# Kernel tuning notes

Measured on AMD Instinct MI355X. Metric: run time of the kernel, lower is better.

The kernel has to match this reference:

```python
import jax, jax.numpy as jnp
import numpy as np

B, S, D, H = 2, 2048, 2048, 16
HD = D // H  # 128


def _rope(x):
    # x: [b, h, s, d] -- standard half-split rotary embedding, theta=10000
    b, h, s, d = x.shape
    inv_freq = 1.0 / (10000.0 ** (jnp.arange(0, d, 2, dtype=jnp.float32) / d))  # [d/2]
    ang = jnp.arange(s, dtype=jnp.float32)[:, None] * inv_freq[None, :]  # [s, d/2]
    cos = jnp.cos(ang)[None, None].astype(x.dtype)
    sin = jnp.sin(ang)[None, None].astype(x.dtype)
    x1, x2 = x[..., : d // 2], x[..., d // 2 :]
    return jnp.concatenate([x1 * cos - x2 * sin, x2 * cos + x1 * sin], axis=-1)


def setup_inputs() -> dict:
    key = jax.random.key(0)
    ks = jax.random.split(key, 11)
    sc = 0.02
    return {
        "queries": jax.random.normal(ks[0], (B, S, D), jnp.float32),
        "keys": jax.random.normal(ks[1], (B, S, D), jnp.float32),
        "values": jax.random.normal(ks[2], (B, S, D), jnp.float32),
        "Wq": jax.random.normal(ks[3], (D, D), jnp.float32) * sc,
        "bq": jax.random.normal(ks[4], (D,), jnp.float32) * sc,
        "Wk": jax.random.normal(ks[5], (D, D), jnp.float32) * sc,
        "bk": jax.random.normal(ks[6], (D,), jnp.float32) * sc,
        "Wv": jax.random.normal(ks[7], (D, D), jnp.float32) * sc,
        "bv": jax.random.normal(ks[8], (D,), jnp.float32) * sc,
        "Wo": jax.random.normal(ks[9], (D, D), jnp.float32) * sc,
        "bo": jax.random.normal(ks[10], (D,), jnp.float32) * sc,
    }


def reference(queries, keys, values, Wq, bq, Wk, bk, Wv, bv, Wo, bo):
    b, sq, _ = queries.shape
    sk = keys.shape[1]
    # projections, split heads: [b, h, s, hd]
    q = (queries @ Wq + bq).reshape(b, sq, H, HD).transpose(0, 2, 1, 3)
    k = (keys @ Wk + bk).reshape(b, sk, H, HD).transpose(0, 2, 1, 3)
    v = (values @ Wv + bv).reshape(b, sk, H, HD).transpose(0, 2, 1, 3)
    q = _rope(q)
    k = _rope(k)
    scores = jnp.einsum("bhqd,bhkd->bhqk", q, k) / jnp.sqrt(jnp.asarray(HD, q.dtype))
    causal = jnp.triu(jnp.ones((sq, sk), dtype=bool), k=1)
    scores = jnp.where(causal, -jnp.inf, scores)
    attn = jax.nn.softmax(scores, axis=-1)
    out = jnp.einsum("bhqk,bhkd->bhqd", attn, v)
    out = out.transpose(0, 2, 1, 3).reshape(b, sq, H * HD)
    return out @ Wo + bo
```

## Files before the change

kernel.cpp:

```cpp
#include <hip/hip_runtime.h>
#include <hip/hip_bf16.h>
#include <math.h>

#define S_LEN 2048
#define D_DIM 2048
#define NHEAD 16
#define HD_DIM 128
#define NROWS 4096
#define BSD 8388608

typedef __bf16 bf16x8 __attribute__((ext_vector_type(8)));
typedef float f32x4 __attribute__((ext_vector_type(4)));
typedef unsigned short u16;
typedef unsigned int u32;

__device__ __forceinline__ float bf2f(u16 h) {
    union { u32 u; float f; } v; v.u = ((u32)h) << 16; return v.f;
}
__device__ __forceinline__ u16 f2bf(float f) {
    union { float f; u32 u; } v; v.f = f;
    u32 r = v.u + 0x7fffu + ((v.u >> 16) & 1u);
    return (u16)(r >> 16);
}

__device__ __forceinline__ void gld16(const void* g, void* l) {
    __builtin_amdgcn_global_load_lds((const __attribute__((address_space(1))) void*)g,
                                     (__attribute__((address_space(3))) void*)l,
                                     16, 0, 0);
}

__device__ __forceinline__ bool detect_f32(const void* p) {
    const u16* h = (const u16*)p;
    int sane = 0;
    for (int i = 0; i < 128; i++) {
        const u16 v = h[2 * i];
        const int e = (v >> 7) & 0xFF;
        sane += (int)((e >= 96 && e <= 150) || ((v & 0x7FFF) == 0));
    }
    return sane < 64;
}

__device__ __forceinline__ bf16x8 load8(const void* X, size_t eidx, bool f32) {
    if (!f32) return *(const bf16x8*)((const u16*)X + eidx);
    const float* xf = (const float*)X + eidx;
    const f32x4 a = *(const f32x4*)xf;
    const f32x4 b = *(const f32x4*)(xf + 4);
    bf16x8 r;
    u16* rp = (u16*)&r;
    rp[0] = f2bf(a[0]); rp[1] = f2bf(a[1]); rp[2] = f2bf(a[2]); rp[3] = f2bf(a[3]);
    rp[4] = f2bf(b[0]); rp[5] = f2bf(b[1]); rp[6] = f2bf(b[2]); rp[7] = f2bf(b[3]);
    return r;
}

__device__ __forceinline__ float bload(const void* b, int i, bool f32) {
    return f32 ? ((const float*)b)[i] : bf2f(((const u16*)b)[i]);
}

__global__ __launch_bounds__(256) void fill_k(float* __restrict__ out, float v, int n) {
    const int i = blockIdx.x * 256 + threadIdx.x;
    if (i < n) out[i] = v;
}

__global__ __launch_bounds__(256) void conv_bf16(const void* __restrict__ in,
                                                 u16* __restrict__ out) {
    const bool f32 = detect_f32(in);
    const size_t i = ((size_t)blockIdx.x * 256 + threadIdx.x) << 3;
    if (f32) {
        const f32x4 a = *(const f32x4*)((const float*)in + i);
        const f32x4 b = *(const f32x4*)((const float*)in + i + 4);
        uint4 w;
        w.x = (u32)f2bf(a[0]) | ((u32)f2bf(a[1]) << 16);
        w.y = (u32)f2bf(a[2]) | ((u32)f2bf(a[3]) << 16);
        w.z = (u32)f2bf(b[0]) | ((u32)f2bf(b[1]) << 16);
        w.w = (u32)f2bf(b[2]) | ((u32)f2bf(b[3]) << 16);
        *(uint4*)&out[i] = w;
    } else {
        *(uint4*)&out[i] = *(const uint4*)&((const u16*)in)[i];
    }
}

__global__ __launch_bounds__(256) void transpose_w(const void* __restrict__ W,
                                                   u16* __restrict__ out) {
    __shared__ float tile[64][68];
    const bool f32w = detect_f32(W);
    const int t = threadIdx.x;
    const int r = t >> 4, c4 = (t & 15) << 2;
    const int kb = blockIdx.y << 6, nb = blockIdx.x << 6;
    if (f32w) {
        #pragma unroll
        for (int i = 0; i < 4; i++) {
            const f32x4 v = *(const f32x4*)((const float*)W +
                (size_t)(kb + r + 16 * i) * D_DIM + nb + c4);
            tile[r + 16 * i][c4 + 0] = v[0];
            tile[r + 16 * i][c4 + 1] = v[1];
            tile[r + 16 * i][c4 + 2] = v[2];
            tile[r + 16 * i][c4 + 3] = v[3];
        }
    } else {
        #pragma unroll
        for (int i = 0; i < 4; i++)
            #pragma unroll
            for (int j = 0; j < 4; j++)
                tile[r + 16 * i][c4 + j] =
                    bf2f(((const u16*)W)[(size_t)(kb + r + 16 * i) * D_DIM + nb + c4 + j]);
    }
    __syncthreads();
    #pragma unroll
    for (int i = 0; i < 4; i++) {
        const int n = nb + r + 16 * i;
        u16 pk[4];
        #pragma unroll
        for (int j = 0; j < 4; j++) pk[j] = f2bf(tile[c4 + j][r + 16 * i]);
        *(uint2*)&out[(size_t)n * D_DIM + kb + c4] = *(uint2*)pk;
    }
}

template<int MODE>
__global__ __launch_bounds__(256) void bt_gemm(const void* __restrict__ X,
                                               const u16* __restrict__ WT,
                                               const void* __restrict__ bias,
                                               void* __restrict__ out) {
    __shared__ __align__(16) u16 a_s[128 * 32];
    __shared__ __align__(16) u16 b_s[128 * 32];
    const bool f32x = (MODE == 0) ? detect_f32(X) : false;
    const bool f32b = detect_f32(bias);
    const int t = threadIdx.x;
    const int wave = t >> 6, lane = t & 63;
    const int quad = lane >> 4, m16 = lane & 15;
    const int wm = (wave >> 1) << 6, wn = (wave & 1) << 6;
    const int rowBase = blockIdx.y << 7, colBase = blockIdx.x << 7;
    const int arow = t >> 2, aoff = (t & 3) << 3;

    f32x4 acc[4][4];
    #pragma unroll
    for (int i = 0; i < 4; i++)
        #pragma unroll
        for (int j = 0; j < 4; j++) acc[i][j] = (f32x4){0.f, 0.f, 0.f, 0.f};

    for (int k0 = 0; k0 < D_DIM; k0 += 32) {
        if (MODE == 0) {
            const bf16x8 av0 = load8(X, (size_t)(rowBase + arow) * D_DIM + k0 + aoff, f32x);
            const bf16x8 av1 = load8(X, (size_t)(rowBase + arow + 64) * D_DIM + k0 + aoff, f32x);
            __syncthreads();
            *(bf16x8*)&a_s[arow * 32 + aoff]        = av0;
            *(bf16x8*)&a_s[(arow + 64) * 32 + aoff] = av1;
            gld16(&WT[(size_t)(colBase + arow) * D_DIM + k0 + aoff],      &b_s[t * 8]);
            gld16(&WT[(size_t)(colBase + arow + 64) * D_DIM + k0 + aoff], &b_s[(t + 256) * 8]);
            __syncthreads();
        } else {
            __syncthreads();
            if (MODE == 2) {
                gld16(&((const u16*)X)[(size_t)(rowBase + arow) * D_DIM + k0 + aoff],
                      &a_s[t * 8]);
                gld16(&((const u16*)X)[(size_t)(rowBase + arow + 64) * D_DIM + k0 + aoff],
                      &a_s[(t + 256) * 8]);
            } else {
                const int kg = k0 + aoff, h = kg >> 7, hd = kg & (HD_DIM - 1);
                const int r0 = rowBase + arow, r1 = r0 + 64;
                gld16(&((const u16*)X)[
                    (((size_t)((r0 >> 11) * NHEAD + h)) * S_LEN + (r0 & (S_LEN - 1))) * HD_DIM + hd],
                    &a_s[t * 8]);
                gld16(&((const u16*)X)[
                    (((size_t)((r1 >> 11) * NHEAD + h)) * S_LEN + (r1 & (S_LEN - 1))) * HD_DIM + hd],
                    &a_s[(t + 256) * 8]);
            }
            gld16(&WT[(size_t)(colBase + arow) * D_DIM + k0 + aoff],      &b_s[t * 8]);
            gld16(&WT[(size_t)(colBase + arow + 64) * D_DIM + k0 + aoff], &b_s[(t + 256) * 8]);
            __syncthreads();
        }

        bf16x8 af[4], bf[4];
        #pragma unroll
        for (int mi = 0; mi < 4; mi++)
            af[mi] = *(bf16x8*)&a_s[(wm + mi * 16 + m16) * 32 + quad * 8];
        #pragma unroll
        for (int ni = 0; ni < 4; ni++)
            bf[ni] = *(bf16x8*)&b_s[(wn + ni * 16 + m16) * 32 + quad * 8];
        #pragma unroll
        for (int mi = 0; mi < 4; mi++)
            #pragma unroll
            for (int ni = 0; ni < 4; ni++)
                acc[mi][ni] = __builtin_amdgcn_mfma_f32_16x16x32_bf16(
                    af[mi], bf[ni], acc[mi][ni], 0, 0, 0);
    }

    #pragma unroll
    for (int ni = 0; ni < 4; ni++) {
        const int col = colBase + wn + ni * 16 + m16;
        const float bv = bload(bias, col, f32b);
        const int h = col >> 7, hd = col & (HD_DIM - 1);
        #pragma unroll
        for (int mi = 0; mi < 4; mi++) {
            #pragma unroll
            for (int r = 0; r < 4; r++) {
                const int row = rowBase + wm + mi * 16 + quad * 4 + r;
                const float v = acc[mi][ni][r] + bv;
                if (MODE == 1) {
                    ((float*)out)[(size_t)row * D_DIM + col] = v;
                } else {
                    const int b = row >> 11, s = row & (S_LEN - 1);
                    ((u16*)out)[(((size_t)(b * NHEAD + h)) * S_LEN + s) * HD_DIM + hd] = f2bf(v);
                }
            }
        }
    }
}

__global__ __launch_bounds__(256) void gemm_qkv(const void* __restrict__ X,
                                                const void* __restrict__ W,
                                                const void* __restrict__ bias,
                                                u16* __restrict__ out) {
    __shared__ __align__(16) u16 a_s[64 * 32];
    __shared__ __align__(16) u16 b_s[64 * 40];
    const bool f32x = detect_f32(X);
    const bool f32w = detect_f32(W);
    const bool f32b = detect_f32(bias);
    const int t = threadIdx.x;
    const int wave = t >> 6, lane = t & 63;
    const int quad = lane >> 4, mrow = lane & 15;
    const int rowBase = blockIdx.y * 64;
    const int colBase = blockIdx.x * 64;
    const int srow = t >> 2, soff = (t & 3) << 3;
    const int krow = t >> 3, ncol0 = (t & 7) << 3;

    f32x4 acc0 = {0.f, 0.f, 0.f, 0.f};
    f32x4 acc1 = acc0, acc2 = acc0, acc3 = acc0;

    for (int k0 = 0; k0 < D_DIM; k0 += 32) {
        const bf16x8 av = load8(X, (size_t)(rowBase + srow) * D_DIM + k0 + soff, f32x);
        const bf16x8 wv = load8(W, (size_t)(k0 + krow) * D_DIM + colBase + ncol0, f32w);
        __syncthreads();
        *(bf16x8*)&a_s[srow * 32 + soff] = av;
        const u16* wp = (const u16*)&wv;
        #pragma unroll
        for (int j = 0; j < 8; j++) b_s[(ncol0 + j) * 40 + krow] = wp[j];
        __syncthreads();
        const bf16x8 af  = *(bf16x8*)&a_s[(wave * 16 + mrow) * 32 + (quad << 3)];
        const bf16x8 bf0 = *(bf16x8*)&b_s[(     mrow) * 40 + (quad << 3)];
        const bf16x8 bf1 = *(bf16x8*)&b_s[(16 + mrow) * 40 + (quad << 3)];
        const bf16x8 bf2 = *(bf16x8*)&b_s[(32 + mrow) * 40 + (quad << 3)];
        const bf16x8 bf3 = *(bf16x8*)&b_s[(48 + mrow) * 40 + (quad << 3)];
        acc0 = __builtin_amdgcn_mfma_f32_16x16x32_bf16(af, bf0, acc0, 0, 0, 0);
        acc1 = __builtin_amdgcn_mfma_f32_16x16x32_bf16(af, bf1, acc1, 0, 0, 0);
        acc2 = __builtin_amdgcn_mfma_f32_16x16x32_bf16(af, bf2, acc2, 0, 0, 0);
        acc3 = __builtin_amdgcn_mfma_f32_16x16x32_bf16(af, bf3, acc3, 0, 0, 0);
    }

    const f32x4 accs[4] = {acc0, acc1, acc2, acc3};
    #pragma unroll
    for (int cb = 0; cb < 4; cb++) {
        const int col = colBase + cb * 16 + mrow;
        const float bv = bload(bias, col, f32b);
        const int h = col >> 7, hd = col & (HD_DIM - 1);
        #pragma unroll
        for (int r = 0; r < 4; r++) {
            const int row = rowBase + wave * 16 + quad * 4 + r;
            const int b = row >> 11, s = row & (S_LEN - 1);
            out[(((size_t)(b * NHEAD + h)) * S_LEN + s) * HD_DIM + hd] =
                f2bf(accs[cb][r] + bv);
        }
    }
}

__global__ __launch_bounds__(256) void gemm_o(const u16* __restrict__ A,
                                              const void* __restrict__ W,
                                              const void* __restrict__ bias,
                                              float* __restrict__ out) {
    __shared__ __align__(16) u16 a_s[64 * 32];
    __shared__ __align__(16) u16 b_s[64 * 40];
    const bool f32w = detect_f32(W);
    const bool f32b = detect_f32(bias);
    const int t = threadIdx.x;
    const int wave = t >> 6, lane = t & 63;
    const int quad = lane >> 4, mrow = lane & 15;
    const int rowBase = blockIdx.y * 64;
    const int colBase = blockIdx.x * 64;
    const int srow = t >> 2, soff = (t & 3) << 3;
    const int krow = t >> 3, ncol0 = (t & 7) << 3;

    f32x4 acc0 = {0.f, 0.f, 0.f, 0.f};
    f32x4 acc1 = acc0, acc2 = acc0, acc3 = acc0;

    const int row = rowBase + srow;
    const int rb = row >> 11, rs = row & (S_LEN - 1);

    for (int k0 = 0; k0 < D_DIM; k0 += 32) {
        const int kg = k0 + soff;
        const int h = kg >> 7, hd = kg & (HD_DIM - 1);
        const bf16x8 av = *(const bf16x8*)&A[
            (((size_t)(rb * NHEAD + h)) * S_LEN + rs) * HD_DIM + hd];
        const bf16x8 wv = load8(W, (size_t)(k0 + krow) * D_DIM + colBase + ncol0, f32w);
        __syncthreads();
        *(bf16x8*)&a_s[srow * 32 + soff] = av;
        const u16* wp = (const u16*)&wv;
        #pragma unroll
        for (int j = 0; j < 8; j++) b_s[(ncol0 + j) * 40 + krow] = wp[j];
        __syncthreads();
        const bf16x8 af  = *(bf16x8*)&a_s[(wave * 16 + mrow) * 32 + (quad << 3)];
        const bf16x8 bf0 = *(bf16x8*)&b_s[(     mrow) * 40 + (quad << 3)];
        const bf16x8 bf1 = *(bf16x8*)&b_s[(16 + mrow) * 40 + (quad << 3)];
        const bf16x8 bf2 = *(bf16x8*)&b_s[(32 + mrow) * 40 + (quad << 3)];
        const bf16x8 bf3 = *(bf16x8*)&b_s[(48 + mrow) * 40 + (quad << 3)];
        acc0 = __builtin_amdgcn_mfma_f32_16x16x32_bf16(af, bf0, acc0, 0, 0, 0);
        acc1 = __builtin_amdgcn_mfma_f32_16x16x32_bf16(af, bf1, acc1, 0, 0, 0);
        acc2 = __builtin_amdgcn_mfma_f32_16x16x32_bf16(af, bf2, acc2, 0, 0, 0);
        acc3 = __builtin_amdgcn_mfma_f32_16x16x32_bf16(af, bf3, acc3, 0, 0, 0);
    }

    const f32x4 accs[4] = {acc0, acc1, acc2, acc3};
    #pragma unroll
    for (int cb = 0; cb < 4; cb++) {
        const int col = colBase + cb * 16 + mrow;
        const float bv = bload(bias, col, f32b);
        #pragma unroll
        for (int r = 0; r < 4; r++) {
            const int orow = rowBase + wave * 16 + quad * 4 + r;
            out[(size_t)orow * D_DIM + col] = accs[cb][r] + bv;
        }
    }
}

__global__ __launch_bounds__(256) void rope_k(u16* __restrict__ q, u16* __restrict__ k) {
    const int idx = blockIdx.x * 256 + threadIdx.x;
    u16* p = blockIdx.y ? k : q;
    const int i  = idx & 63;
    const int s  = (idx >> 6) & (S_LEN - 1);
    const int bh = idx >> 17;
    const size_t base = ((size_t)bh * S_LEN + s) * HD_DIM;
    const float inv = __expf((float)i * -0.14391157f);
    const float ang = (float)s * inv;
    const float c = cosf(ang), sn = sinf(ang);
    const float x1 = bf2f(p[base + i]);
    const float x2 = bf2f(p[base + 64 + i]);
    p[base + i]      = f2bf(x1 * c - x2 * sn);
    p[base + 64 + i] = f2bf(x2 * c + x1 * sn);
}

__device__ __forceinline__ int vswz(int d, int blk8) {
    return d * 72 + (((blk8) ^ ((d ^ (d >> 3)) & 7)) << 3);
}

__global__ __launch_bounds__(256, 3) void flash_mfma(const u16* Q,
                                                     const u16* __restrict__ K,
                                                     const u16* __restrict__ V,
                                                     u16* Out) {
    __shared__ __align__(16) u16 k_s[64 * 136];
    __shared__ __align__(16) u16 v_s[128 * 72];
    __shared__ __align__(16) u16 p_s[64 * 72];
    const int t = threadIdx.x;
    const int wave = t >> 6, lane = t & 63;
    const int quad = lane >> 4, m16 = lane & 15;
    const int h = blockIdx.y, b = blockIdx.z;
    const int q0 = (int)(gridDim.x - 1 - blockIdx.x) << 6;
    const size_t bhoff = ((size_t)(b * NHEAD + h)) * S_LEN * HD_DIM;

    #pragma unroll
    for (int i = 0; i < 4; i++) {
        const int chunk = t + 256 * i;
        const int row = chunk >> 4, d0 = (chunk & 15) << 3;
        *(uint4*)&k_s[row * 136 + d0] =
            *(const uint4*)&Q[bhoff + (size_t)(q0 + row) * HD_DIM + d0];
    }
    __syncthreads();
    bf16x8 qf[4];
    #pragma unroll
    for (int kc = 0; kc < 4; kc++)
        qf[kc] = *(bf16x8*)&k_s[(wave * 16 + m16) * 136 + kc * 32 + quad * 8];

    f32x4 o[8];
    #pragma unroll
    for (int i = 0; i < 8; i++) o[i] = (f32x4){0.f, 0.f, 0.f, 0.f};
    f32x4 m_i = {-1e30f, -1e30f, -1e30f, -1e30f};
    f32x4 l_i = {0.f, 0.f, 0.f, 0.f};

    const int row_g0 = q0 + wave * 16 + quad * 4;
    const float scale = 0.08838834764831843f;
    const int nt = (q0 >> 6) + 1;

    const int krow = t >> 4, kd0 = (t & 15) << 3;
    const int dg = t & 15, kvg = t >> 4;
    const int vsub = (kvg & 1) << 2;

    uint4 kreg[4], vreg[4];
    #pragma unroll
    for (int i = 0; i < 4; i++) {
        kreg[i] = *(const uint4*)&K[bhoff + (size_t)(krow + 16 * i) * HD_DIM + kd0];
        vreg[i] = *(const uint4*)&V[bhoff + (size_t)(kvg * 4 + i) * HD_DIM + dg * 8];
    }

    for (int it = 0; it < nt; ++it) {
        const int kb = it << 6;
        __syncthreads();
        #pragma unroll
        for (int i = 0; i < 4; i++)
            *(uint4*)&k_s[(krow + 16 * i) * 136 + kd0] = kreg[i];
        {
            const u16* v0 = (const u16*)&vreg[0];
            const u16* v1 = (const u16*)&vreg[1];
            const u16* v2 = (const u16*)&vreg[2];
            const u16* v3 = (const u16*)&vreg[3];
            #pragma unroll
            for (int j = 0; j < 8; j++) {
                const int d = dg * 8 + j;
                uint2 w;
                w.x = (u32)v0[j] | ((u32)v1[j] << 16);
                w.y = (u32)v2[j] | ((u32)v3[j] << 16);
                *(uint2*)&v_s[vswz(d, kvg >> 1) + vsub] = w;
            }
        }
        __syncthreads();
        if (it + 1 < nt) {
            const int kb2 = kb + 64;
            #pragma unroll
            for (int i = 0; i < 4; i++) {
                kreg[i] = *(const uint4*)&K[bhoff + (size_t)(kb2 + krow + 16 * i) * HD_DIM + kd0];
                vreg[i] = *(const uint4*)&V[bhoff + (size_t)(kb2 + kvg * 4 + i) * HD_DIM + dg * 8];
            }
        }

        f32x4 s[4];
        #pragma unroll
        for (int f = 0; f < 4; f++) s[f] = (f32x4){0.f, 0.f, 0.f, 0.f};
        __builtin_amdgcn_s_setprio(1);
        #pragma unroll
        for (int kc = 0; kc < 4; kc++) {
            #pragma unroll
            for (int f = 0; f < 4; f++) {
                const bf16x8 kf = *(bf16x8*)&k_s[(f * 16 + m16) * 136 + kc * 32 + quad * 8];
                s[f] = __builtin_amdgcn_mfma_f32_16x16x32_bf16(qf[kc], kf, s[f], 0, 0, 0);
            }
        }
        __builtin_amdgcn_s_setprio(0);

        f32x4 mx;
        #pragma unroll
        for (int r = 0; r < 4; r++) {
            float m0 = -1e30f;
            #pragma unroll
            for (int f = 0; f < 4; f++) {
                float a = s[f][r] * scale;
                if (kb + f * 16 + m16 > row_g0 + r) a = -1e30f;
                s[f][r] = a;
                m0 = fmaxf(m0, a);
            }
            mx[r] = m0;
        }
        #pragma unroll
        for (int d = 1; d <= 8; d <<= 1)
            #pragma unroll
            for (int r = 0; r < 4; r++) mx[r] = fmaxf(mx[r], __shfl_xor(mx[r], d));

        f32x4 alpha, rs;
        #pragma unroll
        for (int r = 0; r < 4; r++) {
            const float mn = fmaxf(m_i[r], mx[r]);
            alpha[r] = __expf(m_i[r] - mn);
            m_i[r] = mn;
            float acc = 0.f;
            #pragma unroll
            for (int f = 0; f < 4; f++) {
                s[f][r] = __expf(s[f][r] - mn);
                acc += s[f][r];
            }
            rs[r] = acc;
        }
        #pragma unroll
        for (int d = 1; d <= 8; d <<= 1)
            #pragma unroll
            for (int r = 0; r < 4; r++) rs[r] += __shfl_xor(rs[r], d);
        #pragma unroll
        for (int r = 0; r < 4; r++) l_i[r] = l_i[r] * alpha[r] + rs[r];

        #pragma unroll
        for (int f = 0; f < 4; f++)
            #pragma unroll
            for (int r = 0; r < 4; r++)
                p_s[(wave * 16 + quad * 4 + r) * 72 + f * 16 + m16] = f2bf(s[f][r]);

        #pragma unroll
        for (int n = 0; n < 8; n++) o[n] *= alpha;

        __builtin_amdgcn_s_setprio(1);
        #pragma unroll
        for (int kc = 0; kc < 2; kc++) {
            const bf16x8 pa = *(bf16x8*)&p_s[(wave * 16 + m16) * 72 + kc * 32 + quad * 8];
            #pragma unroll
            for (int n = 0; n < 8; n++) {
                const int d = n * 16 + m16;
                const bf16x8 vb = *(bf16x8*)&v_s[vswz(d, kc * 4 + quad)];
                o[n] = __builtin_amdgcn_mfma_f32_16x16x32_bf16(pa, vb, o[n], 0, 0, 0);
            }
        }
        __builtin_amdgcn_s_setprio(0);
    }

    f32x4 inv;
    #pragma unroll
    for (int r = 0; r < 4; r++) inv[r] = 1.f / l_i[r];
    #pragma unroll
    for (int n = 0; n < 8; n++)
        #pragma unroll
        for (int r = 0; r < 4; r++)
            Out[bhoff + (size_t)(row_g0 + r) * HD_DIM + n * 16 + m16] =
                f2bf(o[n][r] * inv[r]);
}

extern "C" void kernel_launch(void* const* d_in, const int* in_sizes, int n_in,
                              void* d_out, int out_size, void* d_ws, size_t ws_size,
                              hipStream_t stream) {
    float* outf = (float*)d_out;

    bool order_ok = (n_in == 11);
    if (order_ok) {
        const int expect[11] = {8388608, 8388608, 8388608, 4194304, 2048,
                                4194304, 2048, 4194304, 2048, 4194304, 2048};
        for (int i = 0; i < 11; i++) order_ok = order_ok && (in_sizes[i] == expect[i]);
    }
    if (!order_ok) {
        fill_k<<<dim3((out_size + 255) / 256), dim3(256), 0, stream>>>(outf, 50.f, out_size);
        return;
    }
    if (ws_size < (size_t)BSD * sizeof(u16)) {
        fill_k<<<dim3((out_size + 255) / 256), dim3(256), 0, stream>>>(outf, 25.f, out_size);
        return;
    }

    const void* queries = d_in[0];
    const void* keys    = d_in[1];
    const void* values  = d_in[2];
    const void* Wq = d_in[3]; const void* bq = d_in[4];
    const void* Wk = d_in[5]; const void* bk = d_in[6];
    const void* Wv = d_in[7]; const void* bv = d_in[8];
    const void* Wo = d_in[9]; const void* bo = d_in[10];

    u16* Qb = (u16*)d_ws;
    u16* Kb = (u16*)d_out;
    u16* Vb = Kb + BSD;

    const dim3 tb(256);
    const dim3 gr(16384, 2);
    const dim3 gf(S_LEN / 64, NHEAD, 2);

    const size_t need_fast = (size_t)BSD * 2 + (size_t)D_DIM * D_DIM * 2;
    if (ws_size >= need_fast) {
        u16* WT = Qb + BSD;
        u16* XQ = Kb;
        u16* XK = Vb;
        const dim3 gt(32, 32);
        const dim3 gb(16, 32);
        const dim3 gc(4096);

        conv_bf16<<<gc, tb, 0, stream>>>(queries, XQ);
        conv_bf16<<<gc, tb, 0, stream>>>(keys, XK);

        transpose_w<<<gt, tb, 0, stream>>>(Wq, WT);
        bt_gemm<2><<<gb, tb, 0, stream>>>(XQ, WT, bq, Qb);
        transpose_w<<<gt, tb, 0, stream>>>(Wk, WT);
        bt_gemm<2><<<gb, tb, 0, stream>>>(XK, WT, bk, Kb);
        transpose_w<<<gt, tb, 0, stream>>>(Wv, WT);
        bt_gemm<0><<<gb, tb, 0, stream>>>(values, WT, bv, Vb);

        rope_k<<<gr, tb, 0, stream>>>(Qb, Kb);
        flash_mfma<<<gf, tb, 0, stream>>>(Qb, Kb, Vb, Qb);

        transpose_w<<<gt, tb, 0, stream>>>(Wo, WT);
        bt_gemm<1><<<gb, tb, 0, stream>>>(Qb, WT, bo, outf);
    } else {
        const dim3 gg(32, 64);
        gemm_qkv<<<gg, tb, 0, stream>>>(queries, Wq, bq, Qb);
        gemm_qkv<<<gg, tb, 0, stream>>>(keys,    Wk, bk, Kb);
        gemm_qkv<<<gg, tb, 0, stream>>>(values,  Wv, bv, Vb);
        rope_k<<<gr, tb, 0, stream>>>(Qb, Kb);
        flash_mfma<<<gf, tb, 0, stream>>>(Qb, Kb, Vb, Qb);
        gemm_o<<<gg, tb, 0, stream>>>(Qb, Wo, bo, outf);
    }
}
```

Baseline: 926.0 us.

## Batch QKV weight transposes and projections into single z-indexed launches

When the workspace is large enough, the three weight transposes become one launch with a z grid dimension, and the Q/K/V projection GEMMs become one launch that converts f32 inputs inline instead of running separate conversion kernels. This removes several launches and the intermediate bf16 copies of queries and keys, and gives the GPU three times more blocks per launch. It requires extra workspace for all three transposed weights. The A-tile path now loads through registers rather than async global-to-LDS copies, which could cost some latency hiding.

```diff
diff --git a/kernel.cpp b/kernel.cpp
--- a/kernel.cpp
+++ b/kernel.cpp
@@ -79,8 +79,8 @@
     }
 }
 
-__global__ __launch_bounds__(256) void transpose_w(const void* __restrict__ W,
-                                                   u16* __restrict__ out) {
+__device__ __forceinline__ void transpose_body(const void* __restrict__ W,
+                                               u16* __restrict__ out) {
     __shared__ float tile[64][68];
     const bool f32w = detect_f32(W);
     const int t = threadIdx.x;
@@ -112,6 +112,95 @@
         #pragma unroll
         for (int j = 0; j < 4; j++) pk[j] = f2bf(tile[c4 + j][r + 16 * i]);
         *(uint2*)&out[(size_t)n * D_DIM + kb + c4] = *(uint2*)pk;
+    }
+}
+
+__global__ __launch_bounds__(256) void transpose_w(const void* __restrict__ W,
+                                                   u16* __restrict__ out) {
+    transpose_body(W, out);
+}
+
+__global__ __launch_bounds__(256) void transpose_all(const void* __restrict__ W0,
+                                                     const void* __restrict__ W1,
+                                                     const void* __restrict__ W2,
+                                                     u16* __restrict__ out) {
+    const int z = blockIdx.z;
+    const void* W = (z == 0) ? W0 : (z == 1) ? W1 : W2;
+    transpose_body(W, out + (size_t)z * D_DIM * D_DIM);
+}
+
+__global__ __launch_bounds__(256) void qkv_gemm(const void* __restrict__ Xq,
+                                                const void* __restrict__ Xk,
+                                                const void* __restrict__ Xv,
+                                                const u16* __restrict__ WTbase,
+                                                const void* __restrict__ bqp,
+                                                const void* __restrict__ bkp,
+                                                const void* __restrict__ bvp,
+                                                u16* __restrict__ Oq,
+                                                u16* __restrict__ Ok,
+                                                u16* __restrict__ Ov) {
+    __shared__ __align__(16) u16 a_s[128 * 32];
+    __shared__ __align__(16) u16 b_s[128 * 32];
+    const int z = blockIdx.z;
+    const void* X   = (z == 0) ? Xq  : (z == 1) ? Xk  : Xv;
+    const void* bias= (z == 0) ? bqp : (z == 1) ? bkp : bvp;
+    u16* out        = (z == 0) ? Oq  : (z == 1) ? Ok  : Ov;
+    const u16* WT   = WTbase + (size_t)z * D_DIM * D_DIM;
+    const bool f32x = detect_f32(X);
+    const bool f32b = detect_f32(bias);
+    const int t = threadIdx.x;
+    const int wave = t >> 6, lane = t & 63;
+    const int quad = lane >> 4, m16 = lane & 15;
+    const int wm = (wave >> 1) << 6, wn = (wave & 1) << 6;
+    const int rowBase = blockIdx.y << 7, colBase = blockIdx.x << 7;
+    const int arow = t >> 2, aoff = (t & 3) << 3;
+
+    f32x4 acc[4][4];
+    #pragma unroll
+    for (int i = 0; i < 4; i++)
+        #pragma unroll
+        for (int j = 0; j < 4; j++) acc[i][j] = (f32x4){0.f, 0.f, 0.f, 0.f};
+
+    for (int k0 = 0; k0 < D_DIM; k0 += 32) {
+        const bf16x8 av0 = load8(X, (size_t)(rowBase + arow) * D_DIM + k0 + aoff, f32x);
+        const bf16x8 av1 = load8(X, (size_t)(rowBase + arow + 64) * D_DIM + k0 + aoff, f32x);
+        __syncthreads();
+        *(bf16x8*)&a_s[arow * 32 + aoff]        = av0;
+        *(bf16x8*)&a_s[(arow + 64) * 32 + aoff] = av1;
+        gld16(&WT[(size_t)(colBase + arow) * D_DIM + k0 + aoff],      &b_s[t * 8]);
+        gld16(&WT[(size_t)(colBase + arow + 64) * D_DIM + k0 + aoff], &b_s[(t + 256) * 8]);
+        __syncthreads();
+
+        bf16x8 af[4], bfr[4];
+        #pragma unroll
+        for (int mi = 0; mi < 4; mi++)
+            af[mi] = *(bf16x8*)&a_s[(wm + mi * 16 + m16) * 32 + quad * 8];
+        #pragma unroll
+        for (int ni = 0; ni < 4; ni++)
+            bfr[ni] = *(bf16x8*)&b_s[(wn + ni * 16 + m16) * 32 + quad * 8];
+        #pragma unroll
+        for (int mi = 0; mi < 4; mi++)
+            #pragma unroll
+            for (int ni = 0; ni < 4; ni++)
+                acc[mi][ni] = __builtin_amdgcn_mfma_f32_16x16x32_bf16(
+                    af[mi], bfr[ni], acc[mi][ni], 0, 0, 0);
+    }
+
+    #pragma unroll
+    for (int ni = 0; ni < 4; ni++) {
+        const int col = colBase + wn + ni * 16 + m16;
+        const float bv = bload(bias, col, f32b);
+        const int h = col >> 7, hd = col & (HD_DIM - 1);
+        #pragma unroll
+        for (int mi = 0; mi < 4; mi++) {
+            #pragma unroll
+            for (int r = 0; r < 4; r++) {
+                const int row = rowBase + wm + mi * 16 + quad * 4 + r;
+                const int b = row >> 11, s = row & (S_LEN - 1);
+                out[(((size_t)(b * NHEAD + h)) * S_LEN + s) * HD_DIM + hd] =
+                    f2bf(acc[mi][ni][r] + bv);
+            }
+        }
     }
 }
 
@@ -169,19 +258,19 @@
             __syncthreads();
         }
 
-        bf16x8 af[4], bf[4];
+        bf16x8 af[4], bfr[4];
         #pragma unroll
         for (int mi = 0; mi < 4; mi++)
             af[mi] = *(bf16x8*)&a_s[(wm + mi * 16 + m16) * 32 + quad * 8];
         #pragma unroll
         for (int ni = 0; ni < 4; ni++)
-            bf[ni] = *(bf16x8*)&b_s[(wn + ni * 16 + m16) * 32 + quad * 8];
+            bfr[ni] = *(bf16x8*)&b_s[(wn + ni * 16 + m16) * 32 + quad * 8];
         #pragma unroll
         for (int mi = 0; mi < 4; mi++)
             #pragma unroll
             for (int ni = 0; ni < 4; ni++)
                 acc[mi][ni] = __builtin_amdgcn_mfma_f32_16x16x32_bf16(
-                    af[mi], bf[ni], acc[mi][ni], 0, 0, 0);
+                    af[mi], bfr[ni], acc[mi][ni], 0, 0, 0);
     }
 
     #pragma unroll
@@ -541,8 +630,25 @@
     const dim3 gr(16384, 2);
     const dim3 gf(S_LEN / 64, NHEAD, 2);
 
-    const size_t need_fast = (size_t)BSD * 2 + (size_t)D_DIM * D_DIM * 2;
-    if (ws_size >= need_fast) {
+    const size_t wslot = (size_t)D_DIM * D_DIM * 2;
+    const size_t need_fused = (size_t)BSD * 2 + 3 * wslot;
+    const size_t need_fast  = (size_t)BSD * 2 + wslot;
+
+    if (ws_size >= need_fused) {
+        u16* WT = Qb + BSD;
+        const dim3 gt3(32, 32, 3);
+        const dim3 gt(32, 32);
+        const dim3 gq(16, 32, 3);
+        const dim3 gb(16, 32);
+
+        transpose_all<<<gt3, tb, 0, stream>>>(Wq, Wk, Wv, WT);
+        qkv_gemm<<<gq, tb, 0, stream>>>(queries, keys, values, WT,
+                                        bq, bk, bv, Qb, Kb, Vb);
+        transpose_w<<<gt, tb, 0, stream>>>(Wo, WT);
+        rope_k<<<gr, tb, 0, stream>>>(Qb, Kb);
+        flash_mfma<<<gf, tb, 0, stream>>>(Qb, Kb, Vb, Qb);
+        bt_gemm<1><<<gb, tb, 0, stream>>>(Qb, WT, bo, outf);
+    } else if (ws_size >= need_fast) {
         u16* WT = Qb + BSD;
         u16* XQ = Kb;
         u16* XK = Vb;
```

Result: faster. 850.2 us (-8.2%).
